# Performance work log

Measured on AMD Instinct MI355X. Metric: run time of the kernel, lower is better.

The kernel has to match this reference:

```python
import jax, jax.numpy as jnp
import numpy as np

DIM = 512
HEADS = 8
HEAD_DIM = DIM // HEADS
EPS = 1e-5

def _ln(x, g, b):
    m = jnp.mean(x, axis=-1, keepdims=True)
    v = jnp.mean((x - m) ** 2, axis=-1, keepdims=True)
    return (x - m) * jax.lax.rsqrt(v + EPS) * g + b

def setup_inputs() -> dict:
    key = jax.random.key(0)
    ks = jax.random.split(key, 12)
    s = 0.02
    d, dff = DIM, 4 * DIM
    inp = {
        'x': jax.random.normal(ks[0], (8, 4096, d), jnp.float32),
        'Wq': jax.random.normal(ks[1], (d, d), jnp.float32) * s,
        'bq': jnp.zeros((d,), jnp.float32),
        'Wk': jax.random.normal(ks[2], (d, d), jnp.float32) * s,
        'bk': jnp.zeros((d,), jnp.float32),
        'Wv': jax.random.normal(ks[3], (d, d), jnp.float32) * s,
        'bv': jnp.zeros((d,), jnp.float32),
        'Wo': jax.random.normal(ks[4], (d, d), jnp.float32) * s,
        'bo': jnp.zeros((d,), jnp.float32),
        'g1': jnp.ones((d,), jnp.float32),
        'b1': jnp.zeros((d,), jnp.float32),
        'g2': jnp.ones((d,), jnp.float32),
        'b2': jnp.zeros((d,), jnp.float32),
        'Wf1': jax.random.normal(ks[5], (d, dff), jnp.float32) * s,
        'bf1': jnp.zeros((dff,), jnp.float32),
        'Wf2': jax.random.normal(ks[6], (dff, d), jnp.float32) * s,
        'bf2': jnp.zeros((d,), jnp.float32),
    }
    return inp

def _linear_attn(x, Wq, bq, Wk, bk, Wv, bv, Wo, bo):
    b, n, d = x.shape
    def split(t):
        return t.reshape(b, n, HEADS, HEAD_DIM).transpose(0, 2, 1, 3)  # bhnd
    q = split(x @ Wq + bq)
    k = split(x @ Wk + bk)
    v = split(x @ Wv + bv)
    q = jax.nn.elu(q) + 1.0
    k = jax.nn.elu(k) + 1.0
    kv = jnp.einsum('bhnd,bhnf->bhdf', k, v)
    out = jnp.einsum('bhnd,bhdf->bhnf', q, kv)
    out = out.transpose(0, 2, 1, 3).reshape(b, n, d)
    return out @ Wo + bo

def reference(x, Wq, bq, Wk, bk, Wv, bv, Wo, bo, g1, b1, g2, b2, Wf1, bf1, Wf2, bf2):
    # series decomposition: AvgPool1d(k=3, stride=1, pad=1, count_include_pad=True)
    xp = jnp.pad(x, ((0, 0), (1, 1), (0, 0)))
    trend = (xp[:, :-2] + xp[:, 1:-1] + xp[:, 2:]) / 3.0
    seasonal = x - trend
    seasonal = seasonal + _linear_attn(_ln(seasonal, g1, b1), Wq, bq, Wk, bk, Wv, bv, Wo, bo)
    h = _ln(seasonal, g2, b2)
    h = jax.nn.gelu(h @ Wf1 + bf1, approximate=False) @ Wf2 + bf2
    seasonal = seasonal + h
    return seasonal + trend
```

## Files before the change

kernel.cpp:

```cpp
#include <hip/hip_runtime.h>
#include <math.h>

typedef __bf16 bf16;
typedef __attribute__((ext_vector_type(8))) __bf16 bf16x8;
typedef __attribute__((ext_vector_type(4))) float floatx4;

#define DIM 512
#define DFF 2048
#define SEQ 4096
#define ROWS 32768

#define GLOBAL_AS(p) ((const __attribute__((address_space(1))) void*)(p))
#define LDS_AS(p)    ((__attribute__((address_space(3))) void*)(p))

__global__ __launch_bounds__(256) void prep_w_kernel(const float* __restrict__ W,
                                                     bf16* __restrict__ Wt, int K, int N)
{
    int idx = blockIdx.x * 256 + threadIdx.x;
    if (idx >= K * N) return;
    int k = idx % K;
    int n = idx / K;
    Wt[idx] = (bf16)W[(size_t)k * N + n];
}

__global__ __launch_bounds__(256) void pack_bias_kernel(const float* __restrict__ bq,
                                                        const float* __restrict__ bk,
                                                        const float* __restrict__ bv,
                                                        float* __restrict__ out)
{
    int i = blockIdx.x * 256 + threadIdx.x;
    if (i >= 1536) return;
    out[i] = (i < 512) ? bq[i] : (i < 1024 ? bk[i - 512] : bv[i - 1024]);
}

__device__ inline float wave_red(float v)
{
#pragma unroll
    for (int off = 32; off; off >>= 1) v += __shfl_xor(v, off, 64);
    return v;
}

__global__ __launch_bounds__(256) void decomp_ln_kernel(const float* __restrict__ x,
                                                        const float* __restrict__ g,
                                                        const float* __restrict__ be,
                                                        float* __restrict__ S,
                                                        bf16* __restrict__ XN)
{
    int wave = threadIdx.x >> 6, lane = threadIdx.x & 63;
    int r = blockIdx.x * 4 + wave;
    int n = r & (SEQ - 1);
    const float4* xr = (const float4*)(x + (size_t)r * DIM);
    float4 z = make_float4(0.f, 0.f, 0.f, 0.f);
    float s[8];
#pragma unroll
    for (int i = 0; i < 2; ++i) {
        int c4 = lane * 2 + i;
        float4 v0 = xr[c4];
        float4 vm = (n > 0)       ? xr[c4 - DIM / 4] : z;
        float4 vp = (n < SEQ - 1) ? xr[c4 + DIM / 4] : z;
        s[i * 4 + 0] = v0.x - (vm.x + v0.x + vp.x) * (1.f / 3.f);
        s[i * 4 + 1] = v0.y - (vm.y + v0.y + vp.y) * (1.f / 3.f);
        s[i * 4 + 2] = v0.z - (vm.z + v0.z + vp.z) * (1.f / 3.f);
        s[i * 4 + 3] = v0.w - (vm.w + v0.w + vp.w) * (1.f / 3.f);
    }
    float4* Sr = (float4*)(S + (size_t)r * DIM);
    Sr[lane * 2]     = make_float4(s[0], s[1], s[2], s[3]);
    Sr[lane * 2 + 1] = make_float4(s[4], s[5], s[6], s[7]);

    float sum = 0.f;
#pragma unroll
    for (int j = 0; j < 8; ++j) sum += s[j];
    sum = wave_red(sum);
    float mean = sum * (1.f / DIM);
    float vs = 0.f;
#pragma unroll
    for (int j = 0; j < 8; ++j) { float d = s[j] - mean; vs += d * d; }
    vs = wave_red(vs);
    float rstd = rsqrtf(vs * (1.f / DIM) + 1e-5f);

    int c = lane * 8;
    float4 g0 = ((const float4*)(g + c))[0],  g1v = ((const float4*)(g + c))[1];
    float4 b0 = ((const float4*)(be + c))[0], b1v = ((const float4*)(be + c))[1];
    bf16x8 o;
    o[0] = (bf16)((s[0] - mean) * rstd * g0.x + b0.x);
    o[1] = (bf16)((s[1] - mean) * rstd * g0.y + b0.y);
    o[2] = (bf16)((s[2] - mean) * rstd * g0.z + b0.z);
    o[3] = (bf16)((s[3] - mean) * rstd * g0.w + b0.w);
    o[4] = (bf16)((s[4] - mean) * rstd * g1v.x + b1v.x);
    o[5] = (bf16)((s[5] - mean) * rstd * g1v.y + b1v.y);
    o[6] = (bf16)((s[6] - mean) * rstd * g1v.z + b1v.z);
    o[7] = (bf16)((s[7] - mean) * rstd * g1v.w + b1v.w);
    *(bf16x8*)(XN + (size_t)r * DIM + c) = o;
}

__global__ __launch_bounds__(256) void ln_kernel(const float* __restrict__ X,
                                                 const float* __restrict__ g,
                                                 const float* __restrict__ be,
                                                 bf16* __restrict__ XN)
{
    int wave = threadIdx.x >> 6, lane = threadIdx.x & 63;
    int r = blockIdx.x * 4 + wave;
    const float4* xr = (const float4*)(X + (size_t)r * DIM);
    float4 a0 = xr[lane * 2], a1 = xr[lane * 2 + 1];
    float s[8] = {a0.x, a0.y, a0.z, a0.w, a1.x, a1.y, a1.z, a1.w};
    float sum = 0.f;
#pragma unroll
    for (int j = 0; j < 8; ++j) sum += s[j];
    sum = wave_red(sum);
    float mean = sum * (1.f / DIM);
    float vs = 0.f;
#pragma unroll
    for (int j = 0; j < 8; ++j) { float d = s[j] - mean; vs += d * d; }
    vs = wave_red(vs);
    float rstd = rsqrtf(vs * (1.f / DIM) + 1e-5f);
    int c = lane * 8;
    float4 g0 = ((const float4*)(g + c))[0],  g1v = ((const float4*)(g + c))[1];
    float4 b0 = ((const float4*)(be + c))[0], b1v = ((const float4*)(be + c))[1];
    bf16x8 o;
    o[0] = (bf16)((s[0] - mean) * rstd * g0.x + b0.x);
    o[1] = (bf16)((s[1] - mean) * rstd * g0.y + b0.y);
    o[2] = (bf16)((s[2] - mean) * rstd * g0.z + b0.z);
    o[3] = (bf16)((s[3] - mean) * rstd * g0.w + b0.w);
    o[4] = (bf16)((s[4] - mean) * rstd * g1v.x + b1v.x);
    o[5] = (bf16)((s[5] - mean) * rstd * g1v.y + b1v.y);
    o[6] = (bf16)((s[6] - mean) * rstd * g1v.z + b1v.z);
    o[7] = (bf16)((s[7] - mean) * rstd * g1v.w + b1v.w);
    *(bf16x8*)(XN + (size_t)r * DIM + c) = o;
}

enum { M_QKV = 0, M_ATTN = 1, M_FFN1 = 2, M_FFN2 = 3 };

template <int MODE>
__global__ __launch_bounds__(256) void gemm_bt_kernel(const bf16* __restrict__ A, int lda,
                                                      const bf16* __restrict__ Bt,
                                                      const float* __restrict__ bias,
                                                      float* S, const float* __restrict__ X,
                                                      void* Cout, int ldc,
                                                      int N, int K, int rows_per_batch,
                                                      int m_off)
{
    __shared__ __align__(16) bf16 lA[128 * 32];
    __shared__ __align__(16) bf16 lB[128 * 32];
    int tid = threadIdx.x;
    int m0 = blockIdx.y * 128;
    int n0 = blockIdx.x * 128;
    const bf16* Abase = A + (size_t)m0 * lda;
    const bf16* Bbase = Bt + (size_t)n0 * K;
    if (rows_per_batch) Bbase += (size_t)(m0 / rows_per_batch) * (size_t)N * K;

    int lane = tid & 63;
    int wave = tid >> 6;
    int wm = (wave >> 1) * 64;
    int wn = (wave & 1) * 64;
    int lm = lane & 15;
    int quad = lane >> 4;
    int i0w = tid & 192;

    floatx4 acc[4][4];
#pragma unroll
    for (int i = 0; i < 4; ++i)
#pragma unroll
        for (int j = 0; j < 4; ++j) acc[i][j] = (floatx4){0.f, 0.f, 0.f, 0.f};

    for (int k0 = 0; k0 < K; k0 += 32) {
        __syncthreads();
#pragma unroll
        for (int it = 0; it < 2; ++it) {
            int ib = it * 256 + i0w;
            int i  = ib + lane;
            int row = i >> 2;
            int col = (i & 3) * 8;
            __builtin_amdgcn_global_load_lds(GLOBAL_AS(Abase + (size_t)row * lda + k0 + col),
                                             LDS_AS(&lA[ib * 8]), 16, 0, 0);
            __builtin_amdgcn_global_load_lds(GLOBAL_AS(Bbase + (size_t)row * K + k0 + col),
                                             LDS_AS(&lB[ib * 8]), 16, 0, 0);
        }
        __syncthreads();

        bf16x8 af[4], bfv[4];
#pragma unroll
        for (int i = 0; i < 4; ++i)
            af[i] = *(const bf16x8*)&lA[(wm + i * 16 + lm) * 32 + quad * 8];
#pragma unroll
        for (int j = 0; j < 4; ++j)
            bfv[j] = *(const bf16x8*)&lB[(wn + j * 16 + lm) * 32 + quad * 8];
#pragma unroll
        for (int i = 0; i < 4; ++i)
#pragma unroll
            for (int j = 0; j < 4; ++j)
                acc[i][j] = __builtin_amdgcn_mfma_f32_16x16x32_bf16(af[i], bfv[j], acc[i][j], 0, 0, 0);
    }

#pragma unroll
    for (int i = 0; i < 4; ++i) {
        int gm_base = m0 + wm + i * 16 + quad * 4;
#pragma unroll
        for (int j = 0; j < 4; ++j) {
            int gn = n0 + wn + j * 16 + lm;
            float bia = bias[gn];
#pragma unroll
            for (int e = 0; e < 4; ++e) {
                int gm = gm_base + e;
                float val = acc[i][j][e] + bia;
                if constexpr (MODE == M_QKV) {
                    if (gn < 1024) val = (val > 0.f) ? val + 1.f : __expf(val);
                    ((bf16*)Cout)[(size_t)gm * ldc + gn] = (bf16)val;
                } else if constexpr (MODE == M_ATTN) {
                    S[(size_t)gm * DIM + gn] += val;
                } else if constexpr (MODE == M_FFN1) {
                    val = 0.5f * val * (1.f + erff(val * 0.70710678118654752f));
                    ((bf16*)Cout)[(size_t)gm * ldc + gn] = (bf16)val;
                } else {
                    int gmg = m_off + gm;
                    int nn = gmg & (SEQ - 1);
                    size_t o = (size_t)gmg * DIM + gn;
                    float xc = X[o];
                    float xm = (nn > 0)       ? X[o - DIM] : 0.f;
                    float xp = (nn < SEQ - 1) ? X[o + DIM] : 0.f;
                    float* op = (float*)Cout;
                    op[o] = val + op[o] + (xm + xc + xp) * (1.f / 3.f);
                }
            }
        }
    }
}

__global__ __launch_bounds__(256) void kv_mfma_kernel(const bf16* __restrict__ QKV,
                                                      float* __restrict__ KV)
{
    int kc = blockIdx.x, h = blockIdx.y, b = blockIdx.z;
    __shared__ __align__(16) bf16 lbuf[2 * 128 * 64];
    bf16* lk = lbuf;
    bf16* lv = lbuf + 128 * 64;
    int tid = threadIdx.x;
    int lane = tid & 63, wave = tid >> 6;
    int lm = lane & 15, quad = lane >> 4;

    floatx4 acc[4][4];
#pragma unroll
    for (int i = 0; i < 4; ++i)
#pragma unroll
        for (int j = 0; j < 4; ++j) acc[i][j] = (floatx4){0.f, 0.f, 0.f, 0.f};

    const bf16* kb = QKV + (size_t)b * SEQ * 1536 + 512 + (size_t)h * 64;
    const bf16* vb = kb + 512;
    int drow = lane >> 3;
    int d0 = (lane & 7) * 8;

    for (int it = 0; it < 8; ++it) {
        int n0 = kc * 1024 + it * 128;
        __syncthreads();
#pragma unroll
        for (int q = 0; q < 4; ++q) {
            int nbase = wave * 32 + q * 8;
            int ldsoff = wave * 2048 + q * 512;
            __builtin_amdgcn_global_load_lds(GLOBAL_AS(kb + (size_t)(n0 + nbase + drow) * 1536 + d0),
                                             LDS_AS(&lk[ldsoff]), 16, 0, 0);
            __builtin_amdgcn_global_load_lds(GLOBAL_AS(vb + (size_t)(n0 + nbase + drow) * 1536 + d0),
                                             LDS_AS(&lv[ldsoff]), 16, 0, 0);
        }
        __syncthreads();

        int nw = wave * 32 + quad * 8;
        bf16x8 af[4], bfv[4];
#pragma unroll
        for (int i = 0; i < 4; ++i) {
            int dd = i * 16 + lm;
#pragma unroll
            for (int j = 0; j < 8; ++j) af[i][j] = lk[(nw + j) * 64 + dd];
#pragma unroll
            for (int j = 0; j < 8; ++j) bfv[i][j] = lv[(nw + j) * 64 + dd];
        }
#pragma unroll
        for (int i = 0; i < 4; ++i)
#pragma unroll
            for (int j = 0; j < 4; ++j)
                acc[i][j] = __builtin_amdgcn_mfma_f32_16x16x32_bf16(af[i], bfv[j], acc[i][j], 0, 0, 0);
    }

    __syncthreads();
    float* red = (float*)lbuf;
    if (wave < 2) {
#pragma unroll
        for (int i = 0; i < 4; ++i)
#pragma unroll
            for (int j = 0; j < 4; ++j)
#pragma unroll
                for (int e = 0; e < 4; ++e)
                    red[wave * 4096 + (i * 16 + quad * 4 + e) * 64 + j * 16 + lm] = acc[i][j][e];
    }
    __syncthreads();
    if (wave >= 2) {
#pragma unroll
        for (int i = 0; i < 4; ++i)
#pragma unroll
            for (int j = 0; j < 4; ++j)
#pragma unroll
                for (int e = 0; e < 4; ++e)
                    red[(wave - 2) * 4096 + (i * 16 + quad * 4 + e) * 64 + j * 16 + lm] += acc[i][j][e];
    }
    __syncthreads();
    float* dst = KV + ((size_t)kc * 64 + b * 8 + h) * 4096;
#pragma unroll
    for (int p = 0; p < 4; ++p) {
        int e4 = (tid + p * 256) * 4;
        float4 a = *(const float4*)&red[e4];
        float4 c4 = *(const float4*)&red[4096 + e4];
        a.x += c4.x; a.y += c4.y; a.z += c4.z; a.w += c4.w;
        *(float4*)&dst[e4] = a;
    }
}

__global__ __launch_bounds__(256) void kvw_kernel(const float* __restrict__ KV,
                                                  const float* __restrict__ Wo,
                                                  bf16* __restrict__ KVWT)
{
    int jc = blockIdx.x & 7, bh = blockIdx.x >> 3;
    int h = bh & 7, b = bh >> 3;
    __shared__ float skvT[64 * 68];
    int tid = threadIdx.x;
    const float* src = KV + (size_t)bh * 4096;
#pragma unroll
    for (int p = 0; p < 16; ++p) {
        int e = tid + p * 256;
        float s = src[e] + src[e + 262144] + src[e + 524288] + src[e + 786432];
        skvT[(e & 63) * 68 + (e >> 6)] = s;
    }
    __syncthreads();

    int j = tid & 63, dq = tid >> 6;
    int j0 = jc * 64;
    floatx4 acc4[4];
#pragma unroll
    for (int c = 0; c < 4; ++c) acc4[c] = (floatx4){0.f, 0.f, 0.f, 0.f};
    const float* wop = Wo + (size_t)h * 64 * 512 + j0 + j;
#pragma unroll 8
    for (int f = 0; f < 64; ++f) {
        float w = wop[(size_t)f * 512];
        const float* sp = &skvT[f * 68 + dq * 16];
#pragma unroll
        for (int c = 0; c < 4; ++c) {
            floatx4 s = *(const floatx4*)(sp + c * 4);
            acc4[c] += s * w;
        }
    }
    bf16* dst = KVWT + (size_t)b * 262144 + (size_t)(j0 + j) * 512 + h * 64 + dq * 16;
    bf16x8 o0, o1;
#pragma unroll
    for (int t = 0; t < 8; ++t) { o0[t] = (bf16)acc4[t >> 2][t & 3]; o1[t] = (bf16)acc4[2 + (t >> 2)][t & 3]; }
    *(bf16x8*)dst = o0;
    *(bf16x8*)(dst + 8) = o1;
}

extern "C" void kernel_launch(void* const* d_in, const int* in_sizes, int n_in,
                              void* d_out, int out_size, void* d_ws, size_t ws_size,
                              hipStream_t stream)
{
    const float* x   = (const float*)d_in[0];
    const float* Wq  = (const float*)d_in[1];
    const float* bq  = (const float*)d_in[2];
    const float* Wk  = (const float*)d_in[3];
    const float* bk  = (const float*)d_in[4];
    const float* Wv  = (const float*)d_in[5];
    const float* bv  = (const float*)d_in[6];
    const float* Wo  = (const float*)d_in[7];
    const float* bo  = (const float*)d_in[8];
    const float* g1  = (const float*)d_in[9];
    const float* b1  = (const float*)d_in[10];
    const float* g2  = (const float*)d_in[11];
    const float* b2  = (const float*)d_in[12];
    const float* Wf1 = (const float*)d_in[13];
    const float* bf1 = (const float*)d_in[14];
    const float* Wf2 = (const float*)d_in[15];
    const float* bf2 = (const float*)d_in[16];
    float* out = (float*)d_out;
    (void)in_sizes; (void)n_in; (void)out_size; (void)ws_size;

    char* ws = (char*)d_ws;
    size_t off = 0;
    auto alloc = [&](size_t bytes) -> char* {
        char* p = ws + off;
        off += (bytes + 255) & ~(size_t)255;
        return p;
    };
    bf16*  WqkvT = (bf16*)alloc((size_t)1536 * 512 * 2);
    float* bias3 = (float*)alloc(1536 * 4);
    bf16*  Wf1T  = (bf16*)alloc((size_t)2048 * 512 * 2);
    bf16*  Wf2T  = (bf16*)alloc((size_t)512 * 2048 * 2);
    bf16*  XN    = (bf16*)alloc((size_t)ROWS * DIM * 2);
    float* KV    = (float*)alloc((size_t)4 * 64 * 4096 * 4);
    bf16*  KVWT  = (bf16*)alloc((size_t)8 * 512 * 512 * 2);
    bf16*  QKV   = (bf16*)alloc((size_t)ROWS * 1536 * 2);
    bf16*  H1    = QKV;

    prep_w_kernel<<<1024, 256, 0, stream>>>(Wq, WqkvT,              512, 512);
    prep_w_kernel<<<1024, 256, 0, stream>>>(Wk, WqkvT + 512 * 512,  512, 512);
    prep_w_kernel<<<1024, 256, 0, stream>>>(Wv, WqkvT + 1024 * 512, 512, 512);
    prep_w_kernel<<<4096, 256, 0, stream>>>(Wf1, Wf1T, 512, 2048);
    prep_w_kernel<<<4096, 256, 0, stream>>>(Wf2, Wf2T, 2048, 512);
    pack_bias_kernel<<<6, 256, 0, stream>>>(bq, bk, bv, bias3);

    decomp_ln_kernel<<<8192, 256, 0, stream>>>(x, g1, b1, out, XN);

    gemm_bt_kernel<M_QKV><<<dim3(12, 256), 256, 0, stream>>>(
        XN, 512, WqkvT, bias3, nullptr, nullptr, QKV, 1536, 1536, 512, 0, 0);

    kv_mfma_kernel<<<dim3(4, 8, 8), 256, 0, stream>>>(QKV, KV);

    kvw_kernel<<<512, 256, 0, stream>>>(KV, Wo, KVWT);

    gemm_bt_kernel<M_ATTN><<<dim3(4, 256), 256, 0, stream>>>(
        QKV, 1536, KVWT, bo, out, nullptr, nullptr, 0, 512, 512, 4096, 0);

    ln_kernel<<<8192, 256, 0, stream>>>(out, g2, b2, XN);

    for (int c = 0; c < 2; ++c) {
        gemm_bt_kernel<M_FFN1><<<dim3(16, 128), 256, 0, stream>>>(
            XN + (size_t)c * 16384 * 512, 512, Wf1T, bf1, nullptr, nullptr,
            H1, 2048, 2048, 512, 0, 0);
        gemm_bt_kernel<M_FFN2><<<dim3(4, 128), 256, 0, stream>>>(
            H1, 2048, Wf2T, bf2, nullptr, x, out, 512, 512, 2048, 0, c * 16384);
    }
}
```

Baseline: 723.7 us.

## Double-buffer LDS tiles in GEMM and KV kernels and remap workgroups across XCDs

The GEMM and KV-reduction kernels now use two LDS buffers, so the async global-to-LDS load of the next K-tile is issued while MFMAs run on the current tile. This also removes one barrier per iteration. The GEMM additionally remaps workgroup IDs so that consecutive tiles land on the same XCD, aiming for better L2 reuse. In exchange, LDS use per block doubles, which can lower occupancy, and the remap assumes the grid size is divisible by eight.

Result: faster. 677.9 us (-6.3%).

```diff
diff --git a/kernel.cpp b/kernel.cpp
--- a/kernel.cpp
+++ b/kernel.cpp
@@ -139,11 +139,16 @@
                                                       int N, int K, int rows_per_batch,
                                                       int m_off)
 {
-    __shared__ __align__(16) bf16 lA[128 * 32];
-    __shared__ __align__(16) bf16 lB[128 * 32];
+    __shared__ __align__(16) bf16 lA[2][128 * 32];
+    __shared__ __align__(16) bf16 lB[2][128 * 32];
     int tid = threadIdx.x;
-    int m0 = blockIdx.y * 128;
-    int n0 = blockIdx.x * 128;
+
+    int nwg = gridDim.x * gridDim.y;
+    int orig = blockIdx.y * gridDim.x + blockIdx.x;
+    int wg = (orig & 7) * (nwg >> 3) + (orig >> 3);
+    int m0 = (wg / gridDim.x) * 128;
+    int n0 = (wg % gridDim.x) * 128;
+
     const bf16* Abase = A + (size_t)m0 * lda;
     const bf16* Bbase = Bt + (size_t)n0 * K;
     if (rows_per_batch) Bbase += (size_t)(m0 / rows_per_batch) * (size_t)N * K;
@@ -162,8 +167,7 @@
 #pragma unroll
         for (int j = 0; j < 4; ++j) acc[i][j] = (floatx4){0.f, 0.f, 0.f, 0.f};
 
-    for (int k0 = 0; k0 < K; k0 += 32) {
-        __syncthreads();
+    auto stage = [&](int buf, int k0) {
 #pragma unroll
         for (int it = 0; it < 2; ++it) {
             int ib = it * 256 + i0w;
@@ -171,24 +175,30 @@
             int row = i >> 2;
             int col = (i & 3) * 8;
             __builtin_amdgcn_global_load_lds(GLOBAL_AS(Abase + (size_t)row * lda + k0 + col),
-                                             LDS_AS(&lA[ib * 8]), 16, 0, 0);
+                                             LDS_AS(&lA[buf][ib * 8]), 16, 0, 0);
             __builtin_amdgcn_global_load_lds(GLOBAL_AS(Bbase + (size_t)row * K + k0 + col),
-                                             LDS_AS(&lB[ib * 8]), 16, 0, 0);
+                                             LDS_AS(&lB[buf][ib * 8]), 16, 0, 0);
         }
+    };
+
+    stage(0, 0);
+    int cur = 0;
+    for (int k0 = 0; k0 < K; k0 += 32) {
         __syncthreads();
-
+        if (k0 + 32 < K) stage(cur ^ 1, k0 + 32);
         bf16x8 af[4], bfv[4];
 #pragma unroll
         for (int i = 0; i < 4; ++i)
-            af[i] = *(const bf16x8*)&lA[(wm + i * 16 + lm) * 32 + quad * 8];
+            af[i] = *(const bf16x8*)&lA[cur][(wm + i * 16 + lm) * 32 + quad * 8];
 #pragma unroll
         for (int j = 0; j < 4; ++j)
-            bfv[j] = *(const bf16x8*)&lB[(wn + j * 16 + lm) * 32 + quad * 8];
+            bfv[j] = *(const bf16x8*)&lB[cur][(wn + j * 16 + lm) * 32 + quad * 8];
 #pragma unroll
         for (int i = 0; i < 4; ++i)
 #pragma unroll
             for (int j = 0; j < 4; ++j)
                 acc[i][j] = __builtin_amdgcn_mfma_f32_16x16x32_bf16(af[i], bfv[j], acc[i][j], 0, 0, 0);
+        cur ^= 1;
     }
 
 #pragma unroll
@@ -229,9 +239,7 @@
                                                       float* __restrict__ KV)
 {
     int kc = blockIdx.x, h = blockIdx.y, b = blockIdx.z;
-    __shared__ __align__(16) bf16 lbuf[2 * 128 * 64];
-    bf16* lk = lbuf;
-    bf16* lv = lbuf + 128 * 64;
+    __shared__ __align__(16) bf16 lbuf[2][2 * 128 * 64];
     int tid = threadIdx.x;
     int lane = tid & 63, wave = tid >> 6;
     int lm = lane & 15, quad = lane >> 4;
@@ -247,19 +255,26 @@
     int drow = lane >> 3;
     int d0 = (lane & 7) * 8;
 
-    for (int it = 0; it < 8; ++it) {
+    auto stage = [&](int buf, int it) {
         int n0 = kc * 1024 + it * 128;
-        __syncthreads();
 #pragma unroll
         for (int q = 0; q < 4; ++q) {
             int nbase = wave * 32 + q * 8;
             int ldsoff = wave * 2048 + q * 512;
             __builtin_amdgcn_global_load_lds(GLOBAL_AS(kb + (size_t)(n0 + nbase + drow) * 1536 + d0),
-                                             LDS_AS(&lk[ldsoff]), 16, 0, 0);
+                                             LDS_AS(&lbuf[buf][ldsoff]), 16, 0, 0);
             __builtin_amdgcn_global_load_lds(GLOBAL_AS(vb + (size_t)(n0 + nbase + drow) * 1536 + d0),
-                                             LDS_AS(&lv[ldsoff]), 16, 0, 0);
+                                             LDS_AS(&lbuf[buf][8192 + ldsoff]), 16, 0, 0);
         }
+    };
+
+    stage(0, 0);
+    int cur = 0;
+    for (int it = 0; it < 8; ++it) {
         __syncthreads();
+        if (it < 7) stage(cur ^ 1, it + 1);
+        const bf16* lk = lbuf[cur];
+        const bf16* lv = lbuf[cur] + 8192;
 
         int nw = wave * 32 + quad * 8;
         bf16x8 af[4], bfv[4];
@@ -276,6 +291,7 @@
 #pragma unroll
             for (int j = 0; j < 4; ++j)
                 acc[i][j] = __builtin_amdgcn_mfma_f32_16x16x32_bf16(af[i], bfv[j], acc[i][j], 0, 0, 0);
+        cur ^= 1;
     }
 
     __syncthreads();
```
